# Optimization experiments

Hardware: AMD Instinct MI355X
Metric: run time of the kernel (lower is better)

Reference implementation:

```python
import jax, jax.numpy as jnp
import numpy as np

B, T = 128, 512
IN, Z, H, E, TR = 88, 80, 400, 100, 200


def setup_inputs() -> dict:
    key = jax.random.key(0)
    ks = jax.random.split(key, 16)
    r = lambda i, shape: (0.05 * jax.random.normal(ks[i], shape)).astype(jnp.float32)
    z32 = lambda n: jnp.zeros((n,), dtype=jnp.float32)
    return dict(
        mini_batch=jax.random.uniform(ks[0], (B, T, IN), dtype=jnp.float32),
        eps=jax.random.normal(ks[1], (B, T, Z), dtype=jnp.float32),
        W_ih=r(2, (H, IN)), W_hh=r(3, (H, H)), b_ih=z32(H), b_hh=z32(H),
        h0=z32(H), z0=z32(Z),
        W_loc=r(4, (Z, H)), b_loc=z32(Z), W_scale=r(5, (Z, H)), b_scale=z32(Z),
        gW1=r(6, (TR, Z)), gb1=z32(TR), gW2=r(7, (Z, TR)), gb2=z32(Z),
        pW1=r(8, (TR, Z)), pb1=z32(TR), pW2=r(9, (Z, TR)), pb2=z32(Z),
        sW=r(10, (Z, Z)), sb=z32(Z),
        lW=jnp.eye(Z, dtype=jnp.float32), lb=z32(Z),  # lin_z_to_loc initialized to identity in torch code
        eW1=r(11, (E, Z)), eb1=z32(E), eW2=r(12, (E, E)), eb2=z32(E),
        eW3=r(13, (IN, E)), eb3=z32(IN),
    )


def reference(mini_batch, eps, W_ih, W_hh, b_ih, b_hh, h0, z0,
              W_loc, b_loc, W_scale, b_scale,
              gW1, gb1, gW2, gb2, pW1, pb1, pW2, pb2, sW, sb, lW, lb,
              eW1, eb1, eW2, eb2, eW3, eb3):
    Bb = mini_batch.shape[0]
    # --- guide: Elman RNN (relu) over time-reversed input, then reverse back ---
    xr = mini_batch[:, ::-1, :]                          # [B,T,IN]
    pre = jnp.einsum('bti,hi->bth', xr, W_ih) + b_ih     # [B,T,H] input projection precomputed

    def step(h, p):                                      # h:[B,H], p:[B,H]
        h = jax.nn.relu(p + h @ W_hh.T + b_hh)
        return h, h

    h_init = jnp.broadcast_to(h0, (Bb, h0.shape[0]))
    _, hs = jax.lax.scan(step, h_init, jnp.swapaxes(pre, 0, 1))  # hs:[T,B,H]
    rnn_out = jnp.swapaxes(hs, 0, 1)[:, ::-1, :]         # pad_and_reverse (full-length seqs)

    # --- Combiner (meanfield): q(z_t) params, reparameterized sample ---
    z_loc = rnn_out @ W_loc.T + b_loc                    # [B,T,Z]
    z_scale = jax.nn.softplus(rnn_out @ W_scale.T + b_scale)
    z = z_loc + z_scale * eps                            # rsample

    # --- model: GatedTransition on shifted z ---
    z_shift = jnp.concatenate([jnp.broadcast_to(z0, (Bb, 1, z0.shape[0])), z[:, :-1]], axis=1)
    gate = jax.nn.sigmoid(jax.nn.relu(z_shift @ gW1.T + gb1) @ gW2.T + gb2)
    prop = jax.nn.relu(z_shift @ pW1.T + pb1) @ pW2.T + pb2
    trans_loc = (1.0 - gate) * (z_shift @ lW.T + lb) + gate * prop
    trans_scale = jax.nn.softplus(jax.nn.relu(prop) @ sW.T + sb)

    # --- Emitter: p(x_t | z_t) ---
    h1 = jax.nn.relu(z @ eW1.T + eb1)
    h2 = jax.nn.relu(h1 @ eW2.T + eb2)
    emis = jax.nn.sigmoid(h2 @ eW3.T + eb3)              # [B,T,IN]

    return jnp.concatenate([emis, trans_loc, trans_scale], axis=-1)  # [B,T,IN+2Z]
```

## Files before the change

### kernel.cpp

```cpp
#include <hip/hip_runtime.h>
#include <math.h>

typedef unsigned int uint;

constexpr int BB  = 128;
constexpr int TT  = 512;
constexpr int DIN = 88;
constexpr int DZ  = 80;
constexpr int DH  = 400;
constexpr int DE  = 100;
constexpr int DTR = 200;
constexpr int DOUT = DIN + DZ + DZ;

typedef __attribute__((ext_vector_type(8))) short bf16x8;
typedef __attribute__((ext_vector_type(4))) float f32x4;
typedef __attribute__((ext_vector_type(4))) uint  u32x4;
union FU { u32x4 u; bf16x8 v; };

__device__ __forceinline__ float softplusf(float x) {
    return fmaxf(x, 0.f) + log1pf(__expf(-fabsf(x)));
}
__device__ __forceinline__ float sigmoidf(float x) {
    return 1.f / (1.f + __expf(-x));
}
__device__ __forceinline__ uint bf16rn(float f) {
    uint u = __float_as_uint(f);
    return (u + 0x7FFFu + ((u >> 16) & 1u)) >> 16;
}
__device__ __forceinline__ uint pk2(float lo, float hi) {
    return bf16rn(lo) | (bf16rn(hi) << 16);
}
__device__ __forceinline__ bf16x8 fragF32(const float* p) {
    float4 f0 = *(const float4*)p, f1 = *(const float4*)(p + 4);
    FU fu;
    fu.u.x = pk2(f0.x, f0.y); fu.u.y = pk2(f0.z, f0.w);
    fu.u.z = pk2(f1.x, f1.y); fu.u.w = pk2(f1.z, f1.w);
    return fu.v;
}
__device__ __forceinline__ bf16x8 fragF32relu(const float* p) {
    float4 f0 = *(const float4*)p, f1 = *(const float4*)(p + 4);
    FU fu;
    fu.u.x = pk2(fmaxf(f0.x, 0.f), fmaxf(f0.y, 0.f));
    fu.u.y = pk2(fmaxf(f0.z, 0.f), fmaxf(f0.w, 0.f));
    fu.u.z = pk2(fmaxf(f1.x, 0.f), fmaxf(f1.y, 0.f));
    fu.u.w = pk2(fmaxf(f1.z, 0.f), fmaxf(f1.w, 0.f));
    return fu.v;
}
#define MFMA(A, B, C) __builtin_amdgcn_mfma_f32_16x16x32_bf16((A), (B), (C), 0, 0, 0)

struct Srcs { const float* p[13]; };

__global__ __launch_bounds__(256) void packall_kernel(Srcs s, uint* __restrict__ dst) {
    constexpr int O_[13]   = {80,80,200,200,80,80,80,80,100,100,88,400,400};
    constexpr int K_[13]   = {400,400,80,80,200,200,80,80,80,100,100,88,400};
    constexpr int KS_[13]  = {13,13,3,3,7,7,3,3,3,4,4,3,13};
    constexpr int OFF_[13] = {0,65,130,169,208,243,278,293,308,332,364,388,463};
    int tile = blockIdx.x;
    int e = 0;
    #pragma unroll
    for (int i = 1; i < 13; ++i) if (tile >= OFF_[i]) e = i;
    int lt = tile - OFF_[e];
    int nt = lt / KS_[e], ks = lt % KS_[e];
    const float* W = s.p[e];
    int r = threadIdx.x, l = r >> 2, d = r & 3;
    int o = nt * 16 + (l & 15);
    int k = ks * 32 + ((l >> 4) << 3) + 2 * d;
    uint lo = 0, hi = 0;
    if (o < O_[e] && k < K_[e])     lo = bf16rn(W[o * K_[e] + k]);
    if (o < O_[e] && k + 1 < K_[e]) hi = bf16rn(W[o * K_[e] + k + 1]);
    dst[(size_t)tile * 256 + r] = lo | (hi << 16);
}

constexpr int WHH = 463;

__global__ __launch_bounds__(256) void pre_kernel(
    const float* __restrict__ x, const uint* __restrict__ bt,
    const float* __restrict__ b_ih, const float* __restrict__ b_hh,
    float* __restrict__ pre) {
    __shared__ float xs[16 * 100];
    const int b = blockIdx.y, tt0 = blockIdx.x * 16, tid = threadIdx.x;
    const int l = tid & 63, wid = tid >> 6, lr = l & 15, lg = l >> 4;
    for (int idx = tid; idx < 1600; idx += 256) {
        int r = idx / 100, k = idx % 100;
        xs[idx] = (k < DIN) ? x[((size_t)b * TT + (TT - 1 - (tt0 + r))) * DIN + k] : 0.f;
    }
    __syncthreads();
    bf16x8 af[3];
    #pragma unroll
    for (int ks = 0; ks < 3; ++ks) af[ks] = fragF32(xs + lr * 100 + ks * 32 + lg * 8);
    const uint4* bt4 = (const uint4*)bt;
    for (int nt = wid; nt < 25; nt += 4) {
        f32x4 acc = {0.f, 0.f, 0.f, 0.f};
        const uint4* bp = bt4 + (size_t)(388 + nt * 3) * 64 + l;
        #pragma unroll
        for (int ks = 0; ks < 3; ++ks) { FU bu; bu.u = *(const u32x4*)(bp + ks * 64); acc = MFMA(af[ks], bu.v, acc); }
        int col = nt * 16 + lr;
        float bias = b_ih[col] + b_hh[col];
        #pragma unroll
        for (int i = 0; i < 4; ++i)
            pre[((size_t)b * TT + tt0 + lg * 4 + i) * DH + col] = acc[i] + bias;
    }
}

__global__ __launch_bounds__(512) __attribute__((amdgpu_waves_per_eu(2, 2)))
void rnn_kernel(const u32x4* __restrict__ bt4, const float* __restrict__ h0,
                float* __restrict__ prehs) {
    extern __shared__ char smem[];
    uint*  hb   = (uint*)smem;
    float* pb   = (float*)(smem + 27136);
    u32x4* wt24 = (u32x4*)(smem + 27136 + 51712);

    const int tid = threadIdx.x, lane = tid & 63, wid = tid >> 6;
    const int batch = lane & 15, lg = lane >> 4;
    const int b0 = blockIdx.x * 16;

    u32x4 A0[13], A1[13], A2[13];
    {
        const u32x4* base = bt4 + (size_t)(WHH + 3 * wid * 13) * 64 + lane;
        #pragma unroll
        for (int ks = 0; ks < 13; ++ks) {
            A0[ks] = base[ks * 64];
            A1[ks] = base[(13 + ks) * 64];
            A2[ks] = base[(26 + ks) * 64];
        }
    }
    #pragma unroll
    for (int ks = 0; ks < 13; ++ks)
        asm volatile("" : "+v"(A0[ks]), "+v"(A1[ks]), "+v"(A2[ks]));

    for (int i = tid; i < 13 * 64; i += 512)
        wt24[i] = bt4[(size_t)(WHH + 24 * 13) * 64 + i];

    for (int i = tid; i < 2 * 16 * 12; i += 512) {
        int buf = i / 192, r = i % 192, bs = r / 12, d = 200 + r % 12;
        hb[buf * 3392 + bs * 212 + d] = 0u;
    }
    for (int i = tid; i < 16 * 200; i += 512) {
        int bs = i / 200, d = i % 200;
        hb[bs * 212 + d] = pk2(h0[2 * d], h0[2 * d + 1]);
    }
    {
        const u32x4* ra = (const u32x4*)(prehs + ((size_t)(b0 + 2 * wid) * TT) * DH);
        const u32x4* rb = (const u32x4*)(prehs + ((size_t)(b0 + 2 * wid + 1) * TT) * DH);
        u32x4* wa = (u32x4*)(pb + (2 * wid) * 404);
        u32x4* wb = (u32x4*)(pb + (2 * wid + 1) * 404);
        wa[lane] = ra[lane];
        wb[lane] = rb[lane];
        if (lane < 36) { wa[64 + lane] = ra[64 + lane]; wb[64 + lane] = rb[64 + lane]; }
    }
    __syncthreads();

    uint cur = 0;
    for (int tt = 0; tt < TT; ++tt) {
        u32x4 na0, na1, nb0, nb1;
        const bool hasNext = (tt + 1 < TT);
        if (hasNext) {
            const u32x4* ra = (const u32x4*)(prehs + ((size_t)(b0 + 2 * wid) * TT + tt + 1) * DH);
            const u32x4* rb = (const u32x4*)(prehs + ((size_t)(b0 + 2 * wid + 1) * TT + tt + 1) * DH);
            na0 = ra[lane]; nb0 = rb[lane];
            if (lane < 36) { na1 = ra[64 + lane]; nb1 = rb[64 + lane]; }
        }

        const uint*  hcur = hb + cur * 3392;
        const float* pcur = pb + cur * (16 * 404);
        f32x4 c0 = {0.f, 0.f, 0.f, 0.f}, c1 = c0, c2 = c0, c24 = c0;
        const u32x4* hrow = (const u32x4*)(hcur + batch * 212);
        #pragma unroll
        for (int ks = 0; ks < 13; ++ks) {
            FU b; b.u = hrow[ks * 4 + lg];
            FU a0; a0.u = A0[ks]; c0 = MFMA(a0.v, b.v, c0);
            FU a1; a1.u = A1[ks]; c1 = MFMA(a1.v, b.v, c1);
            FU a2; a2.u = A2[ks]; c2 = MFMA(a2.v, b.v, c2);
            if (wid == 7) { FU w; w.u = wt24[ks * 64 + lane]; c24 = MFMA(w.v, b.v, c24); }
        }

        uint*  hnxt = hb + (cur ^ 1) * 3392;
        float* pnxt = pb + (cur ^ 1) * (16 * 404);
        uint*  grow = (uint*)prehs + ((size_t)(b0 + batch) * TT + tt) * DH;

        #pragma unroll
        for (int s = 0; s < 3; ++s) {
            const int mt = 3 * wid + s;
            f32x4 c = (s == 0) ? c0 : (s == 1) ? c1 : c2;
            float4 pr = *(const float4*)(pcur + batch * 404 + mt * 16 + lg * 4);
            uint d0 = pk2(fmaxf(c[0] + pr.x, 0.f), fmaxf(c[1] + pr.y, 0.f));
            uint d1 = pk2(fmaxf(c[2] + pr.z, 0.f), fmaxf(c[3] + pr.w, 0.f));
            uint2 dd = make_uint2(d0, d1);
            *(uint2*)(hnxt + batch * 212 + mt * 8 + lg * 2) = dd;
            *(uint2*)(grow + mt * 8 + lg * 2) = dd;
        }
        if (wid == 7) {
            float4 pr = *(const float4*)(pcur + batch * 404 + 24 * 16 + lg * 4);
            uint d0 = pk2(fmaxf(c24[0] + pr.x, 0.f), fmaxf(c24[1] + pr.y, 0.f));
            uint d1 = pk2(fmaxf(c24[2] + pr.z, 0.f), fmaxf(c24[3] + pr.w, 0.f));
            uint2 dd = make_uint2(d0, d1);
            *(uint2*)(hnxt + batch * 212 + 24 * 8 + lg * 2) = dd;
            *(uint2*)(grow + 24 * 8 + lg * 2) = dd;
        }

        if (hasNext) {
            u32x4* wa = (u32x4*)(pnxt + (2 * wid) * 404);
            u32x4* wb = (u32x4*)(pnxt + (2 * wid + 1) * 404);
            wa[lane] = na0; wb[lane] = nb0;
            if (lane < 36) { wa[64 + lane] = na1; wb[64 + lane] = nb1; }
        }
        __syncthreads();
        cur ^= 1;
    }
}

__global__ __launch_bounds__(256) void e_kernel(
    const uint4* __restrict__ hs4, const float* __restrict__ eps,
    const float* __restrict__ z0, const uint* __restrict__ bt,
    const float* __restrict__ b_loc, const float* __restrict__ b_scale,
    const float* __restrict__ gb1, const float* __restrict__ pb1,
    const float* __restrict__ gb2, const float* __restrict__ pb2,
    const float* __restrict__ lb,  const float* __restrict__ sb,
    const float* __restrict__ eb1, const float* __restrict__ eb2,
    const float* __restrict__ eb3, float* __restrict__ out) {
    __shared__ float lds[12196];
    float* zl = lds;
    float* AP = lds + 1700;
    float* gp = lds + 8996;

    const int tid = threadIdx.x, l = tid & 63, wid = tid >> 6;
    const int b = blockIdx.y, t0 = blockIdx.x * 16;
    const int lr = l & 15, lg = l >> 4;
    const uint4* bt4 = (const uint4*)bt;

    bf16x8 zf[3];

    {
        const int m0 = (wid >> 1) * 16;
        int r = m0 + lr;
        int t = t0 - 1 + r; t = min(max(t, 0), TT - 1);
        const uint4* rp = hs4 + ((size_t)b * TT + (TT - 1 - t)) * 100;
        bf16x8 af[13];
        FU zz; zz.u = (u32x4){0u, 0u, 0u, 0u};
        #pragma unroll
        for (int ks = 0; ks < 13; ++ks) {
            if (ks == 12 && lg >= 2) af[ks] = zz.v;
            else { FU fu; fu.u = *(const u32x4*)(rp + ks * 4 + lg); af[ks] = fu.v; }
        }
        for (int nt = (wid & 1); nt < 10; nt += 2) {
            f32x4 acc = {0.f, 0.f, 0.f, 0.f};
            const uint4* bp = bt4 + (size_t)(nt * 13) * 64 + l;
            #pragma unroll
            for (int ks = 0; ks < 13; ++ks) { FU bu; bu.u = *(const u32x4*)(bp + ks * 64); acc = MFMA(af[ks], bu.v, acc); }
            int col = nt * 16 + lr;
            float bias = (col < DZ) ? b_loc[col] : b_scale[col - DZ];
            #pragma unroll
            for (int i = 0; i < 4; ++i) {
                int rr = m0 + lg * 4 + i;
                if (rr < 17) AP[rr * 164 + col] = acc[i] + bias;
            }
        }
    }
    __syncthreads();

    for (int idx = tid; idx < 17 * 100; idx += 256) {
        int r = idx / 100, o = idx % 100;
        float zv = 0.f;
        if (o < DZ) {
            int t = t0 - 1 + r;
            if (t < 0) zv = z0[o];
            else {
                float sp = softplusf(AP[r * 164 + DZ + o]);
                zv = AP[r * 164 + o] + sp * eps[((size_t)b * TT + t) * DZ + o];
            }
        }
        zl[idx] = zv;
    }
    __syncthreads();

    {
        #pragma unroll
        for (int ks = 0; ks < 3; ++ks) zf[ks] = fragF32(zl + lr * 100 + ks * 32 + lg * 8);
        for (int idx = tid; idx < 640; idx += 256) {
            int h = idx / 320, rem = idx % 320;
            AP[h * 3648 + (rem / 20) * 228 + 208 + rem % 20] = 0.f;
        }
        for (int nt = wid; nt < 26; nt += 4) {
            f32x4 acc = {0.f, 0.f, 0.f, 0.f};
            const uint4* bp = bt4 + (size_t)(130 + nt * 3) * 64 + l;
            #pragma unroll
            for (int ks = 0; ks < 3; ++ks) { FU bu; bu.u = *(const u32x4*)(bp + ks * 64); acc = MFMA(zf[ks], bu.v, acc); }
            int isP = nt >= 13;
            int col = (isP ? nt - 13 : nt) * 16 + lr;
            float bias = (col < DTR) ? (isP ? pb1[col] : gb1[col]) : 0.f;
            float* dst = AP + isP * 3648;
            #pragma unroll
            for (int i = 0; i < 4; ++i)
                dst[(lg * 4 + i) * 228 + col] = fmaxf(acc[i] + bias, 0.f);
        }
    }
    __syncthreads();

    {
        int half = wid >> 1;
        const float* src = AP + half * 3648;
        bf16x8 apf[7];
        #pragma unroll
        for (int ks = 0; ks < 7; ++ks) apf[ks] = fragF32(src + lr * 228 + ks * 32 + lg * 8);
        for (int idx = tid; idx < 640; idx += 256) {
            int h = idx / 320, rem = idx % 320;
            gp[h * 1600 + (rem / 20) * 100 + 80 + rem % 20] = 0.f;
        }
        for (int nt = (wid & 1); nt < 5; nt += 2) {
            f32x4 acc = {0.f, 0.f, 0.f, 0.f};
            const uint4* bp = bt4 + (size_t)(208 + half * 35 + nt * 7) * 64 + l;
            #pragma unroll
            for (int ks = 0; ks < 7; ++ks) { FU bu; bu.u = *(const u32x4*)(bp + ks * 64); acc = MFMA(apf[ks], bu.v, acc); }
            int col = nt * 16 + lr;
            float bias = half ? pb2[col] : gb2[col];
            float* dst = gp + half * 1600;
            #pragma unroll
            for (int i = 0; i < 4; ++i) {
                float v = acc[i] + bias;
                dst[(lg * 4 + i) * 100 + col] = half ? v : sigmoidf(v);
            }
        }
    }
    __syncthreads();

    {
        bf16x8 z1f[3], prf[3];
        #pragma unroll
        for (int ks = 0; ks < 3; ++ks) {
            z1f[ks] = fragF32(zl + (1 + lr) * 100 + ks * 32 + lg * 8);
            prf[ks] = fragF32relu(gp + 1600 + lr * 100 + ks * 32 + lg * 8);
        }
        for (int tsk = wid; tsk < 18; tsk += 4) {
            if (tsk < 5) {
                f32x4 acc = {0.f, 0.f, 0.f, 0.f};
                const uint4* bp = bt4 + (size_t)(278 + tsk * 3) * 64 + l;
                #pragma unroll
                for (int ks = 0; ks < 3; ++ks) { FU bu; bu.u = *(const u32x4*)(bp + ks * 64); acc = MFMA(zf[ks], bu.v, acc); }
                int col = tsk * 16 + lr;
                float bias = lb[col];
                #pragma unroll
                for (int i = 0; i < 4; ++i) {
                    int rr = lg * 4 + i;
                    float g  = gp[rr * 100 + col];
                    float pv = gp[1600 + rr * 100 + col];
                    out[((size_t)b * TT + t0 + rr) * DOUT + DIN + col] =
                        (1.f - g) * (acc[i] + bias) + g * pv;
                }
            } else if (tsk < 10) {
                int nt = tsk - 5;
                f32x4 acc = {0.f, 0.f, 0.f, 0.f};
                const uint4* bp = bt4 + (size_t)(293 + nt * 3) * 64 + l;
                #pragma unroll
                for (int ks = 0; ks < 3; ++ks) { FU bu; bu.u = *(const u32x4*)(bp + ks * 64); acc = MFMA(prf[ks], bu.v, acc); }
                int col = nt * 16 + lr;
                float bias = sb[col];
                #pragma unroll
                for (int i = 0; i < 4; ++i)
                    out[((size_t)b * TT + t0 + lg * 4 + i) * DOUT + DIN + DZ + col] =
                        softplusf(acc[i] + bias);
            } else {
                int nt = tsk - 10;
                f32x4 acc = {0.f, 0.f, 0.f, 0.f};
                const uint4* bp = bt4 + (size_t)(308 + nt * 3) * 64 + l;
                #pragma unroll
                for (int ks = 0; ks < 3; ++ks) { FU bu; bu.u = *(const u32x4*)(bp + ks * 64); acc = MFMA(z1f[ks], bu.v, acc); }
                int col = nt * 16 + lr;
                float bias = (col < DE) ? eb1[col] : 0.f;
                #pragma unroll
                for (int i = 0; i < 4; ++i)
                    AP[(lg * 4 + i) * 228 + col] = fmaxf(acc[i] + bias, 0.f);
            }
        }
    }
    __syncthreads();

    {
        bf16x8 hf[4];
        #pragma unroll
        for (int ks = 0; ks < 4; ++ks) hf[ks] = fragF32(AP + lr * 228 + ks * 32 + lg * 8);
        for (int nt = wid; nt < 8; nt += 4) {
            f32x4 acc = {0.f, 0.f, 0.f, 0.f};
            const uint4* bp = bt4 + (size_t)(332 + nt * 4) * 64 + l;
            #pragma unroll
            for (int ks = 0; ks < 4; ++ks) { FU bu; bu.u = *(const u32x4*)(bp + ks * 64); acc = MFMA(hf[ks], bu.v, acc); }
            int col = nt * 16 + lr;
            float bias = (col < DE) ? eb2[col] : 0.f;
            #pragma unroll
            for (int i = 0; i < 4; ++i)
                AP[3648 + (lg * 4 + i) * 228 + col] = fmaxf(acc[i] + bias, 0.f);
        }
    }
    __syncthreads();

    {
        bf16x8 hf[4];
        #pragma unroll
        for (int ks = 0; ks < 4; ++ks) hf[ks] = fragF32(AP + 3648 + lr * 228 + ks * 32 + lg * 8);
        for (int nt = wid; nt < 6; nt += 4) {
            f32x4 acc = {0.f, 0.f, 0.f, 0.f};
            const uint4* bp = bt4 + (size_t)(364 + nt * 4) * 64 + l;
            #pragma unroll
            for (int ks = 0; ks < 4; ++ks) { FU bu; bu.u = *(const u32x4*)(bp + ks * 64); acc = MFMA(hf[ks], bu.v, acc); }
            int col = nt * 16 + lr;
            if (col < DIN) {
                float bias = eb3[col];
                #pragma unroll
                for (int i = 0; i < 4; ++i)
                    out[((size_t)b * TT + t0 + lg * 4 + i) * DOUT + col] = sigmoidf(acc[i] + bias);
            }
        }
    }
}

extern "C" void kernel_launch(void* const* d_in, const int* in_sizes, int n_in,
                              void* d_out, int out_size, void* d_ws, size_t ws_size,
                              hipStream_t stream) {
    const float* x       = (const float*)d_in[0];
    const float* eps     = (const float*)d_in[1];
    const float* W_ih    = (const float*)d_in[2];
    const float* W_hh    = (const float*)d_in[3];
    const float* b_ih    = (const float*)d_in[4];
    const float* b_hh    = (const float*)d_in[5];
    const float* h0      = (const float*)d_in[6];
    const float* z0      = (const float*)d_in[7];
    const float* W_loc   = (const float*)d_in[8];
    const float* b_loc   = (const float*)d_in[9];
    const float* W_scale = (const float*)d_in[10];
    const float* b_scale = (const float*)d_in[11];
    const float* gW1 = (const float*)d_in[12];
    const float* gb1 = (const float*)d_in[13];
    const float* gW2 = (const float*)d_in[14];
    const float* gb2 = (const float*)d_in[15];
    const float* pW1 = (const float*)d_in[16];
    const float* pb1 = (const float*)d_in[17];
    const float* pW2 = (const float*)d_in[18];
    const float* pb2 = (const float*)d_in[19];
    const float* sW  = (const float*)d_in[20];
    const float* sb  = (const float*)d_in[21];
    const float* lW  = (const float*)d_in[22];
    const float* lb  = (const float*)d_in[23];
    const float* eW1 = (const float*)d_in[24];
    const float* eb1 = (const float*)d_in[25];
    const float* eW2 = (const float*)d_in[26];
    const float* eb2 = (const float*)d_in[27];
    const float* eW3 = (const float*)d_in[28];
    const float* eb3 = (const float*)d_in[29];

    float* wsf = (float*)d_ws;
    float* prebuf = wsf;
    uint*  bt = (uint*)(wsf + (size_t)BB * TT * DH);

    Srcs s;
    s.p[0] = W_loc;  s.p[1] = W_scale; s.p[2] = gW1; s.p[3] = pW1;
    s.p[4] = gW2;    s.p[5] = pW2;     s.p[6] = lW;  s.p[7] = sW;
    s.p[8] = eW1;    s.p[9] = eW2;     s.p[10] = eW3; s.p[11] = W_ih; s.p[12] = W_hh;
    packall_kernel<<<788, 256, 0, stream>>>(s, bt);

    pre_kernel<<<dim3(TT / 16, BB), 256, 0, stream>>>(x, bt, b_ih, b_hh, prebuf);

    size_t smem = 27136 + 51712 + 13312;
    hipFuncSetAttribute((const void*)rnn_kernel,
                        hipFuncAttributeMaxDynamicSharedMemorySize, (int)smem);
    rnn_kernel<<<dim3(8), dim3(512), smem, stream>>>((const u32x4*)bt, h0, prebuf);

    e_kernel<<<dim3(TT / 16, BB), 256, 0, stream>>>(
        (const uint4*)prebuf, eps, z0, bt,
        b_loc, b_scale, gb1, pb1, gb2, pb2, lb, sb, eb1, eb2, eb3,
        (float*)d_out);
}
```

Measured before the change: 1.130 ms.

## Halve RNN block to 4 waves, each holding 6 W_hh row tiles in registers

The recurrent kernel now runs with 256 threads (4 waves) instead of 512. Each wave keeps six register-resident W_hh tiles instead of three, and the leftover tile moves to wave 0. This lowers the cost of the per-step __syncthreads and spreads more MFMA work per wave to hide latency in the serial time loop. The cost is much higher VGPR pressure (78 u32x4 per lane, 312 VGPRs) with waves_per_eu fixed at 1, which risks spills. Fewer waves are also left to overlap the global prefetch of the next step's pre-activations.

```diff
diff --git a/kernel.cpp b/kernel.cpp
--- a/kernel.cpp
+++ b/kernel.cpp
@@ -2,6 +2,7 @@
 #include <math.h>
 
 typedef unsigned int uint;
+typedef unsigned short ushort;
 
 constexpr int BB  = 128;
 constexpr int TT  = 512;
@@ -102,7 +103,17 @@
     }
 }
 
-__global__ __launch_bounds__(512) __attribute__((amdgpu_waves_per_eu(2, 2)))
+__device__ __forceinline__ void rnn_emit(int mt, f32x4 c, const float* pcur,
+                                         uint* hn, uint* grow, int batch, int lg) {
+    float4 pr = *(const float4*)(pcur + batch * 404 + mt * 16 + lg * 4);
+    uint d0 = pk2(fmaxf(c[0] + pr.x, 0.f), fmaxf(c[1] + pr.y, 0.f));
+    uint d1 = pk2(fmaxf(c[2] + pr.z, 0.f), fmaxf(c[3] + pr.w, 0.f));
+    uint2 dd = make_uint2(d0, d1);
+    *(uint2*)(hn + batch * 212 + mt * 8 + lg * 2) = dd;
+    *(uint2*)(grow + mt * 8 + lg * 2) = dd;
+}
+
+__global__ __launch_bounds__(256) __attribute__((amdgpu_waves_per_eu(1, 1)))
 void rnn_kernel(const u32x4* __restrict__ bt4, const float* __restrict__ h0,
                 float* __restrict__ prehs) {
     extern __shared__ char smem[];
@@ -114,95 +125,94 @@
     const int batch = lane & 15, lg = lane >> 4;
     const int b0 = blockIdx.x * 16;
 
-    u32x4 A0[13], A1[13], A2[13];
-    {
-        const u32x4* base = bt4 + (size_t)(WHH + 3 * wid * 13) * 64 + lane;
-        #pragma unroll
-        for (int ks = 0; ks < 13; ++ks) {
-            A0[ks] = base[ks * 64];
-            A1[ks] = base[(13 + ks) * 64];
-            A2[ks] = base[(26 + ks) * 64];
-        }
-    }
+    u32x4 A[6][13];
     #pragma unroll
-    for (int ks = 0; ks < 13; ++ks)
-        asm volatile("" : "+v"(A0[ks]), "+v"(A1[ks]), "+v"(A2[ks]));
-
-    for (int i = tid; i < 13 * 64; i += 512)
+    for (int s = 0; s < 6; ++s) {
+        const u32x4* base = bt4 + (size_t)(WHH + (wid + 4 * s) * 13) * 64 + lane;
+        #pragma unroll
+        for (int ks = 0; ks < 13; ++ks) A[s][ks] = base[ks * 64];
+    }
+    #pragma unroll
+    for (int s = 0; s < 6; ++s) {
+        #pragma unroll
+        for (int ks = 0; ks < 13; ++ks) asm volatile("" : "+v"(A[s][ks]));
+    }
+
+    for (int i = tid; i < 13 * 64; i += 256)
         wt24[i] = bt4[(size_t)(WHH + 24 * 13) * 64 + i];
-
-    for (int i = tid; i < 2 * 16 * 12; i += 512) {
-        int buf = i / 192, r = i % 192, bs = r / 12, d = 200 + r % 12;
-        hb[buf * 3392 + bs * 212 + d] = 0u;
-    }
-    for (int i = tid; i < 16 * 200; i += 512) {
+    for (int i = tid; i < 2 * 16 * 12; i += 256) {
+        int buf = i / 192, r = i % 192;
+        hb[buf * 3392 + (r / 12) * 212 + 200 + r % 12] = 0u;
+    }
+    for (int i = tid; i < 16 * 200; i += 256) {
         int bs = i / 200, d = i % 200;
         hb[bs * 212 + d] = pk2(h0[2 * d], h0[2 * d + 1]);
     }
-    {
-        const u32x4* ra = (const u32x4*)(prehs + ((size_t)(b0 + 2 * wid) * TT) * DH);
-        const u32x4* rb = (const u32x4*)(prehs + ((size_t)(b0 + 2 * wid + 1) * TT) * DH);
-        u32x4* wa = (u32x4*)(pb + (2 * wid) * 404);
-        u32x4* wb = (u32x4*)(pb + (2 * wid + 1) * 404);
+    #pragma unroll
+    for (int r = 0; r < 4; ++r) {
+        const u32x4* ra = (const u32x4*)(prehs + ((size_t)(b0 + 4 * wid + r) * TT) * DH);
+        u32x4* wa = (u32x4*)(pb + (4 * wid + r) * 404);
         wa[lane] = ra[lane];
-        wb[lane] = rb[lane];
-        if (lane < 36) { wa[64 + lane] = ra[64 + lane]; wb[64 + lane] = rb[64 + lane]; }
+        if (lane < 36) wa[64 + lane] = ra[64 + lane];
     }
     __syncthreads();
 
     uint cur = 0;
     for (int tt = 0; tt < TT; ++tt) {
-        u32x4 na0, na1, nb0, nb1;
+        u32x4 z4 = {0u, 0u, 0u, 0u};
+        u32x4 n0a = z4, n0b = z4, n1a = z4, n1b = z4;
+        u32x4 n2a = z4, n2b = z4, n3a = z4, n3b = z4;
         const bool hasNext = (tt + 1 < TT);
         if (hasNext) {
-            const u32x4* ra = (const u32x4*)(prehs + ((size_t)(b0 + 2 * wid) * TT + tt + 1) * DH);
-            const u32x4* rb = (const u32x4*)(prehs + ((size_t)(b0 + 2 * wid + 1) * TT + tt + 1) * DH);
-            na0 = ra[lane]; nb0 = rb[lane];
-            if (lane < 36) { na1 = ra[64 + lane]; nb1 = rb[64 + lane]; }
+            const u32x4* r0 = (const u32x4*)(prehs + ((size_t)(b0 + 4 * wid + 0) * TT + tt + 1) * DH);
+            const u32x4* r1 = (const u32x4*)(prehs + ((size_t)(b0 + 4 * wid + 1) * TT + tt + 1) * DH);
+            const u32x4* r2 = (const u32x4*)(prehs + ((size_t)(b0 + 4 * wid + 2) * TT + tt + 1) * DH);
+            const u32x4* r3 = (const u32x4*)(prehs + ((size_t)(b0 + 4 * wid + 3) * TT + tt + 1) * DH);
+            n0a = r0[lane]; n1a = r1[lane]; n2a = r2[lane]; n3a = r3[lane];
+            if (lane < 36) {
+                n0b = r0[64 + lane]; n1b = r1[64 + lane];
+                n2b = r2[64 + lane]; n3b = r3[64 + lane];
+            }
         }
 
         const uint*  hcur = hb + cur * 3392;
         const float* pcur = pb + cur * (16 * 404);
-        f32x4 c0 = {0.f, 0.f, 0.f, 0.f}, c1 = c0, c2 = c0, c24 = c0;
+        f32x4 c0 = {0.f, 0.f, 0.f, 0.f}, c1 = c0, c2 = c0, c3 = c0, c4 = c0, c5 = c0, c24 = c0;
         const u32x4* hrow = (const u32x4*)(hcur + batch * 212);
         #pragma unroll
         for (int ks = 0; ks < 13; ++ks) {
             FU b; b.u = hrow[ks * 4 + lg];
-            FU a0; a0.u = A0[ks]; c0 = MFMA(a0.v, b.v, c0);
-            FU a1; a1.u = A1[ks]; c1 = MFMA(a1.v, b.v, c1);
-            FU a2; a2.u = A2[ks]; c2 = MFMA(a2.v, b.v, c2);
-            if (wid == 7) { FU w; w.u = wt24[ks * 64 + lane]; c24 = MFMA(w.v, b.v, c24); }
+            FU a0; a0.u = A[0][ks]; c0 = MFMA(a0.v, b.v, c0);
+            FU a1; a1.u = A[1][ks]; c1 = MFMA(a1.v, b.v, c1);
+            FU a2; a2.u = A[2][ks]; c2 = MFMA(a2.v, b.v, c2);
+            FU a3; a3.u = A[3][ks]; c3 = MFMA(a3.v, b.v, c3);
+            FU a4; a4.u = A[4][ks]; c4 = MFMA(a4.v, b.v, c4);
+            FU a5; a5.u = A[5][ks]; c5 = MFMA(a5.v, b.v, c5);
+            if (wid == 0) { FU w; w.u = wt24[ks * 64 + lane]; c24 = MFMA(w.v, b.v, c24); }
         }
 
         uint*  hnxt = hb + (cur ^ 1) * 3392;
         float* pnxt = pb + (cur ^ 1) * (16 * 404);
         uint*  grow = (uint*)prehs + ((size_t)(b0 + batch) * TT + tt) * DH;
 
-        #pragma unroll
-        for (int s = 0; s < 3; ++s) {
-            const int mt = 3 * wid + s;
-            f32x4 c = (s == 0) ? c0 : (s == 1) ? c1 : c2;
-            float4 pr = *(const float4*)(pcur + batch * 404 + mt * 16 + lg * 4);
-            uint d0 = pk2(fmaxf(c[0] + pr.x, 0.f), fmaxf(c[1] + pr.y, 0.f));
-            uint d1 = pk2(fmaxf(c[2] + pr.z, 0.f), fmaxf(c[3] + pr.w, 0.f));
-            uint2 dd = make_uint2(d0, d1);
-            *(uint2*)(hnxt + batch * 212 + mt * 8 + lg * 2) = dd;
-            *(uint2*)(grow + mt * 8 + lg * 2) = dd;
-        }
-        if (wid == 7) {
-            float4 pr = *(const float4*)(pcur + batch * 404 + 24 * 16 + lg * 4);
-            uint d0 = pk2(fmaxf(c24[0] + pr.x, 0.f), fmaxf(c24[1] + pr.y, 0.f));
-            uint d1 = pk2(fmaxf(c24[2] + pr.z, 0.f), fmaxf(c24[3] + pr.w, 0.f));
-            uint2 dd = make_uint2(d0, d1);
-            *(uint2*)(hnxt + batch * 212 + 24 * 8 + lg * 2) = dd;
-            *(uint2*)(grow + 24 * 8 + lg * 2) = dd;
-        }
+        rnn_emit(wid + 0,  c0, pcur, hnxt, grow, batch, lg);
+        rnn_emit(wid + 4,  c1, pcur, hnxt, grow, batch, lg);
+        rnn_emit(wid + 8,  c2, pcur, hnxt, grow, batch, lg);
+        rnn_emit(wid + 12, c3, pcur, hnxt, grow, batch, lg);
+        rnn_emit(wid + 16, c4, pcur, hnxt, grow, batch, lg);
+        rnn_emit(wid + 20, c5, pcur, hnxt, grow, batch, lg);
+        if (wid == 0) rnn_emit(24, c24, pcur, hnxt, grow, batch, lg);
 
         if (hasNext) {
-            u32x4* wa = (u32x4*)(pnxt + (2 * wid) * 404);
-            u32x4* wb = (u32x4*)(pnxt + (2 * wid + 1) * 404);
-            wa[lane] = na0; wb[lane] = nb0;
-            if (lane < 36) { wa[64 + lane] = na1; wb[64 + lane] = nb1; }
+            u32x4* w0 = (u32x4*)(pnxt + (4 * wid + 0) * 404);
+            u32x4* w1 = (u32x4*)(pnxt + (4 * wid + 1) * 404);
+            u32x4* w2 = (u32x4*)(pnxt + (4 * wid + 2) * 404);
+            u32x4* w3 = (u32x4*)(pnxt + (4 * wid + 3) * 404);
+            w0[lane] = n0a; w1[lane] = n1a; w2[lane] = n2a; w3[lane] = n3a;
+            if (lane < 36) {
+                w0[64 + lane] = n0b; w1[64 + lane] = n1b;
+                w2[64 + lane] = n2b; w3[64 + lane] = n3b;
+            }
         }
         __syncthreads();
         cur ^= 1;
@@ -461,7 +471,7 @@
     size_t smem = 27136 + 51712 + 13312;
     hipFuncSetAttribute((const void*)rnn_kernel,
                         hipFuncAttributeMaxDynamicSharedMemorySize, (int)smem);
-    rnn_kernel<<<dim3(8), dim3(512), smem, stream>>>((const u32x4*)bt, h0, prebuf);
+    rnn_kernel<<<dim3(8), dim3(256), smem, stream>>>((const u32x4*)bt, h0, prebuf);
 
     e_kernel<<<dim3(TT / 16, BB), 256, 0, stream>>>(
         (const uint4*)prebuf, eps, z0, bt,
```

Result: slower. 1.486 ms (+31.5%).
